# Performance work log

Measured on AMD Instinct MI355X. Metric: run time of the kernel, lower is better.

Reference implementation:

```python
import jax, jax.numpy as jnp
import numpy as np
from jax import lax

MID_NODES = 3
EMB = 128
NHID = 64
NHEADS = 8
ALPHA = 0.2
NEG_INF = -9e15


def build_adj(N, mid_nodes):
    # faithful numpy transcription of GATEmbedding.get_adj + row-normalize(adj + I)
    mid = (N - mid_nodes) // 2 + mid_nodes - 1
    width = (N - mid_nodes) // mid_nodes // 2
    A = np.zeros((N, N), dtype=np.float64)
    for i in range(mid_nodes):
        for j in range(N):
            if i == mid_nodes - 1:
                if j > mid_nodes - 1:
                    A[i, j] = 1
            elif j == i + 1 or (j > mid - (i + 1) * width and j < mid + (i + 1) * width):
                A[i, j] = 1
    for i in range(mid_nodes, N):
        for j in range(N):
            if i == mid_nodes:
                if j == mid_nodes + 1:
                    A[i, j] = 1
            elif i == N - 1:
                if j == N - 2:
                    A[i, j] = 1
            elif j == i - 1 or j == i + 1:
                A[i, j] = 1
    A = A + np.eye(N)
    rowsum = A.sum(1)
    r_inv = np.where(rowsum > 0, 1.0 / np.maximum(rowsum, 1e-30), 0.0)
    A = r_inv[:, None] * A
    return jnp.asarray(A, dtype=jnp.float32)


def conv2d(x, w, b):
    y = lax.conv_general_dilated(x, w, (1, 1), 'SAME',
                                 dimension_numbers=('NCHW', 'OIHW', 'NCHW'))
    return y + b[None, :, None, None]


def maxpool2(x):
    return lax.reduce_window(x, -jnp.inf, lax.max, (1, 1, 2, 2), (1, 1, 2, 2), 'VALID')


def slice_cnn(x, w1, b1, w2, b2, w3, b3, w4, b4, fc_w, fc_b):
    x = maxpool2(jax.nn.relu(conv2d(x, w1, b1)))
    x = maxpool2(jax.nn.relu(conv2d(x, w2, b2)))
    x = maxpool2(jax.nn.relu(conv2d(x, w3, b3)))
    x = maxpool2(jax.nn.relu(conv2d(x, w4, b4)))
    x = x.mean(axis=(2, 3))  # [BC,128]
    return x @ fc_w + fc_b


def setup_inputs():
    key = jax.random.key(0)
    ks = jax.random.split(key, 16)
    s = 0.05
    return {
        'input_img': jax.random.normal(ks[0], (8, 16, 128, 128), jnp.float32),
        'w1': jax.random.normal(ks[1], (32, 1, 3, 3), jnp.float32) * s,
        'b1': jnp.zeros((32,), jnp.float32),
        'w2': jax.random.normal(ks[2], (64, 32, 3, 3), jnp.float32) * s,
        'b2': jnp.zeros((64,), jnp.float32),
        'w3': jax.random.normal(ks[3], (128, 64, 3, 3), jnp.float32) * s,
        'b3': jnp.zeros((128,), jnp.float32),
        'w4': jax.random.normal(ks[4], (128, 128, 3, 3), jnp.float32) * s,
        'b4': jnp.zeros((128,), jnp.float32),
        'fc_cnn_w': jax.random.normal(ks[5], (128, EMB), jnp.float32) * s,
        'fc_cnn_b': jnp.zeros((EMB,), jnp.float32),
        'att_W': jax.random.normal(ks[6], (NHEADS, EMB, NHID), jnp.float32) * s,
        'att_a': jax.random.normal(ks[7], (NHEADS, 2 * NHID), jnp.float32) * s,
        'out_W': jax.random.normal(ks[8], (NHID * NHEADS, EMB), jnp.float32) * s,
        'out_a': jax.random.normal(ks[9], (2 * EMB,), jnp.float32) * s,
        'll_w': jax.random.normal(ks[10], (EMB, 2 * EMB), jnp.float32) * s,
        'll_b': jnp.zeros((2 * EMB,), jnp.float32),
        'fc_w': jax.random.normal(ks[11], (2 * EMB, 2), jnp.float32) * s,
        'fc_b': jnp.zeros((2,), jnp.float32),
        'sfc_w': jax.random.normal(ks[12], (EMB, 2), jnp.float32) * s,
        'sfc_b': jnp.zeros((2,), jnp.float32),
    }


def reference(input_img, w1, b1, w2, b2, w3, b3, w4, b4, fc_cnn_w, fc_cnn_b,
              att_W, att_a, out_W, out_a, ll_w, ll_b, fc_w, fc_b, sfc_w, sfc_b):
    B, C, H, W = input_img.shape
    N = C + MID_NODES

    # per-channel CNN embedding, batched over B*C instead of a Python loop
    feats = slice_cnn(input_img.reshape(B * C, 1, H, W),
                      w1, b1, w2, b2, w3, b3, w4, b4, fc_cnn_w, fc_cnn_b)
    feats = feats.reshape(B, C, EMB)                 # slices_features_stack
    slices_hidden = feats.mean(axis=1)               # [B,EMB]
    slices_out = slices_hidden @ sfc_w + sfc_b       # [B,2]

    slices = jnp.zeros((B, N, EMB), feats.dtype).at[:, MID_NODES:, :].set(feats)
    adj = build_adj(N, MID_NODES)                    # [N,N] constant
    mask = (adj > 0)[None, None]                     # [1,1,N,N]

    # multi-head GAT (eval mode: dropout = identity), all heads vectorized
    Wh = jnp.einsum('bnf,kfh->bknh', slices, att_W)  # [B,K,N,NHID]
    a1, a2 = att_a[:, :NHID], att_a[:, NHID:]
    e = jax.nn.leaky_relu(jnp.einsum('bknh,kh->bkn', Wh, a1)[:, :, :, None]
                          + jnp.einsum('bknh,kh->bkn', Wh, a2)[:, :, None, :], ALPHA)
    att = jax.nn.softmax(jnp.where(mask, e, NEG_INF), axis=-1)   # [B,K,N,N]
    batch_attention = att.mean(axis=1)               # [B,N,N]
    h = jnp.einsum('bkij,bkjh->bkih', att, Wh)
    x = jax.nn.elu(h).transpose(0, 2, 1, 3).reshape(B, N, NHEADS * NHID)

    # output GAT layer (concat=False), then external ELU
    Wh2 = x @ out_W                                   # [B,N,EMB]
    oa1, oa2 = out_a[:EMB], out_a[EMB:]
    e2 = jax.nn.leaky_relu((Wh2 @ oa1)[:, :, None] + (Wh2 @ oa2)[:, None, :], ALPHA)
    att2 = jax.nn.softmax(jnp.where(mask[:, 0], e2, NEG_INF), axis=-1)
    image_feature = jax.nn.elu(jnp.einsum('bij,bjh->bih', att2, Wh2))

    image_feature_second = image_feature[:, 0, :]
    image_feature_second = jax.nn.relu(image_feature_second @ ll_w + ll_b)
    prediction = image_feature_second @ fc_w + fc_b
    return (slices_hidden, image_feature_second, prediction, slices_out, batch_attention)
```

## Files before the change

kernel.cpp:

```cpp
#include <hip/hip_runtime.h>
#include <hip/hip_bf16.h>
#include <math.h>


#define NEG_INF_F (-9.0e15f)

typedef __attribute__((ext_vector_type(8))) short frag8;
typedef __attribute__((ext_vector_type(4))) float f32x4;
typedef const __attribute__((address_space(1))) void GasV;
typedef __attribute__((address_space(3))) void LasV;

__device__ __forceinline__ unsigned short f2bf(float f) {
  union { float f; unsigned u; } v; v.f = f;
  unsigned r = v.u + 0x7fffu + ((v.u >> 16) & 1u);
  return (unsigned short)(r >> 16);
}
__device__ __forceinline__ float bf2f(unsigned short u) {
  union { unsigned u; float f; } v; v.u = ((unsigned)u) << 16;
  return v.f;
}

template <int C>
__device__ __forceinline__ int swz(int slot, int px) {
  if constexpr (C == 32) return slot ^ ((px >> 1) & 3);
  else return slot ^ (px & 7);
}

template <int C, int OC>
__device__ __forceinline__ void bprep_dev(const float* __restrict__ w,
                                          unsigned short* __restrict__ bp, int idx) {
  constexpr int CS = C / 32, NSTEP = 9 * CS, NG = (OC / 64) * 2;
  if (idx >= NG * NSTEP * 64 * 2) return;
  int q = idx & 1;
  int lane = (idx >> 1) & 63;
  int gs = idx >> 7;
  int s = gs % NSTEP;
  int g = gs / NSTEP;
  int off = s / CS, c0 = (s % CS) * 32;
  int l15 = lane & 15, l4 = lane >> 4;
  int oc = (g >> 1) * 64 + (g & 1) * 32 + q * 16 + l15;
  int kc = c0 + l4 * 8;
  unsigned short o8[8];
#pragma unroll
  for (int j = 0; j < 8; ++j)
    o8[j] = f2bf(w[((size_t)oc * C + kc + j) * 9 + off]);
  *(uint4*)(bp + (size_t)idx * 8) = *(uint4*)o8;
}

__global__ __launch_bounds__(256) void prep_k(
    const float* __restrict__ w2, const float* __restrict__ w3,
    const float* __restrict__ w4, unsigned short* __restrict__ bp2,
    unsigned short* __restrict__ bp3, unsigned short* __restrict__ bp4,
    float* __restrict__ adj) {
  const int bx = blockIdx.x, t = threadIdx.x;
  if (bx == 0) {
    __shared__ float A[19][19];
    for (int e = t; e < 361; e += 256) {
      int i = e / 19, j = e % 19;
      float v = 0.f;
      const int MIDN = 3, N = 19, MID = 10, WIDTH = 2;
      if (i < MIDN) {
        if (i == MIDN - 1) { if (j > MIDN - 1) v = 1.f; }
        else if (j == i + 1 || (j > MID - (i + 1) * WIDTH && j < MID + (i + 1) * WIDTH)) v = 1.f;
      } else {
        if (i == MIDN) { if (j == MIDN + 1) v = 1.f; }
        else if (i == N - 1) { if (j == N - 2) v = 1.f; }
        else if (j == i - 1 || j == i + 1) v = 1.f;
      }
      if (i == j) v += 1.f;
      A[i][j] = v;
    }
    __syncthreads();
    for (int e = t; e < 361; e += 256) {
      int i = e / 19;
      float rs = 0.f;
      for (int j = 0; j < 19; ++j) rs += A[i][j];
      float rinv = rs > 0.f ? 1.f / rs : 0.f;
      adj[e] = A[i][e % 19] * rinv;
    }
  } else if (bx <= 9) {
    bprep_dev<32, 64>(w2, bp2, (bx - 1) * 256 + t);
  } else if (bx <= 45) {
    bprep_dev<64, 128>(w3, bp3, (bx - 10) * 256 + t);
  } else {
    bprep_dev<128, 128>(w4, bp4, (bx - 46) * 256 + t);
  }
}

__global__ __launch_bounds__(256) void conv12_k(
    const float* __restrict__ in, const float* __restrict__ w1,
    const float* __restrict__ b1, const unsigned short* __restrict__ bprep,
    const float* __restrict__ bias, unsigned short* __restrict__ outH) {
  constexpr int C = 32, OC = 64, W = 64;
  constexpr int PW = W + 2, OH = W / 2;
  constexpr int NSTEP = 9;
  __shared__ float sr[14][132];
  __shared__ __align__(16) unsigned short patchH[6 * PW * C];
  const int t = threadIdx.x;
  const int img = blockIdx.z;
  const int y0 = blockIdx.x * 4;
  const int pr0 = blockIdx.x * 2;
  const size_t out_img = (size_t)img * 34 * 34 * OC;

  const float* ip = in + (size_t)img * 16384;
  for (int e = t; e < 14 * 130; e += 256) {
    int s = e / 130, c = e - s * 130;
    int y = 2 * y0 - 3 + s, x = c - 1;
    sr[s][c] = (y >= 0 && y < 128 && x >= 0 && x < 128) ? ip[y * 128 + x] : 0.f;
  }
  __syncthreads();

  {
    const int px = t & 63, ocg = t >> 6;
    const int gx = px + 1;
    const int ssl = swz<C>(ocg, gx);
    const int ocg_s = __builtin_amdgcn_readfirstlane(ocg);
    const float* wg = w1 + ocg_s * 72;
    const float* bg = b1 + ocg_s * 8;
#pragma unroll
    for (int r = 0; r < 6; ++r) {
      int rp = y0 + r;
      unsigned short h8[8];
      if (rp == 0 || rp == 65) {
#pragma unroll
        for (int i = 0; i < 8; ++i) h8[i] = 0;
      } else {
        float v[4][4];
#pragma unroll
        for (int dy = 0; dy < 4; ++dy)
#pragma unroll
          for (int dx = 0; dx < 4; ++dx) v[dy][dx] = sr[2 * r + dy][2 * px + dx];
#pragma unroll
        for (int i = 0; i < 8; ++i) {
          float m = -1e30f;
#pragma unroll
          for (int dy = 0; dy < 2; ++dy)
#pragma unroll
            for (int dx = 0; dx < 2; ++dx) {
              float a = 0.f;
#pragma unroll
              for (int ky = 0; ky < 3; ++ky)
#pragma unroll
                for (int kx = 0; kx < 3; ++kx)
                  a = fmaf(v[dy + ky][dx + kx], wg[i * 9 + ky * 3 + kx], a);
              m = fmaxf(m, a);
            }
          h8[i] = f2bf(fmaxf(m + bg[i], 0.f));
        }
      }
      *(uint4*)(patchH + (r * PW + gx) * C + ssl * 8) = *(uint4*)h8;
    }
    if (t < 48) {
      int r = t >> 3, rem = t & 7;
      int side = rem >> 2, q = rem & 3;
      const uint4 z4 = {0u, 0u, 0u, 0u};
      *(uint4*)(patchH + (r * PW + side * (PW - 1)) * C + q * 8) = z4;
    }
  }
  __syncthreads();

  const int lane = t & 63, wid = t >> 6;
  const int wm = wid >> 1, wn = wid & 1;
  const int l15 = lane & 15, l4 = lane >> 4;
  const int nbase = wn * 32;
  const unsigned short* bpw = bprep + ((size_t)wn * NSTEP * 64 + lane) * 16;
  const float bb0 = bias[nbase + l15], bb1 = bias[nbase + 16 + l15];

#pragma unroll
  for (int tt = 0; tt < 2; ++tt) {
    f32x4 acc[4][2] = {};
    for (int s = 0; s < NSTEP; ++s) {
      const frag8* bp = (const frag8*)(bpw + (size_t)s * 1024);
      frag8 bh0 = bp[0], bh1 = bp[1];
      const int ky = s / 3, kx = s - ky * 3;
      frag8 ah[4];
#pragma unroll
      for (int f = 0; f < 4; ++f) {
        int m0 = wm * 32 + (f & 1) * 16 + (f >> 1) * 64;
        int ry = m0 / W + 2 * tt + ky;
        int px = (m0 % W) + l15 + kx;
        ah[f] = *(const frag8*)(patchH + ((size_t)ry * PW + px) * C + swz<C>(l4, px) * 8);
      }
#pragma unroll
      for (int f = 0; f < 4; ++f) {
        acc[f][0] = __builtin_amdgcn_mfma_f32_16x16x32_bf16(ah[f], bh0, acc[f][0], 0, 0, 0);
        acc[f][1] = __builtin_amdgcn_mfma_f32_16x16x32_bf16(ah[f], bh1, acc[f][1], 0, 0, 0);
      }
    }
#pragma unroll
    for (int pi = 0; pi < 2; ++pi) {
      const int fa = pi, fb = pi + 2;
      const int pxb = wm * 16 + pi * 8;
#pragma unroll
      for (int n = 0; n < 2; ++n) {
        const float bb = n ? bb1 : bb0;
#pragma unroll
        for (int xp = 0; xp < 2; ++xp) {
          float v = fmaxf(fmaxf(acc[fa][n][2 * xp], acc[fa][n][2 * xp + 1]),
                          fmaxf(acc[fb][n][2 * xp], acc[fb][n][2 * xp + 1]));
          outH[out_img + ((size_t)(pr0 + tt + 1) * 34 + pxb + 2 * l4 + xp + 1) * OC +
               nbase + n * 16 + l15] = f2bf(fmaxf(v + bb, 0.f));
        }
      }
    }
  }

  const uint4 z4 = {0u, 0u, 0u, 0u};
  if (t < 32) {
    int r = t >> 4, side = (t >> 3) & 1, q = t & 7;
    *(uint4*)(outH + out_img + ((size_t)(pr0 + r + 1) * 34 + side * 33) * OC + q * 8) = z4;
  }
  if (pr0 == 0)
    for (int e = t; e < 272; e += 256)
      *(uint4*)(outH + out_img + (size_t)e * 8) = z4;
  if (pr0 + 2 == OH)
    for (int e = t; e < 272; e += 256)
      *(uint4*)(outH + out_img + (size_t)33 * 34 * OC + (size_t)e * 8) = z4;
}

template <int C, int OC, int W, int R, bool PAD = true>
__global__ __launch_bounds__(256) void conv_mfma_k(
    const unsigned short* __restrict__ inH,
    const unsigned short* __restrict__ bprep, const float* __restrict__ bias,
    unsigned short* __restrict__ outH) {
  constexpr int SL = C / 8;
  constexpr int PW = W + 2;
  constexpr int OW = W / 2, OH = W / 2;
  constexpr int PR = R / 2;
  constexpr int CS = C / 32;
  constexpr int NSTEP = 9 * CS;
  constexpr int M = R * W;
  constexpr int MF = M / 32;
  constexpr int E = (R + 2) * PW * SL;
  constexpr int EP = (E + 63) & ~63;
  __shared__ __align__(16) unsigned short patchH[(R + 2) * PW * C + 256];
  const int t = threadIdx.x;
  const int img = blockIdx.z;
  const int y0 = blockIdx.x * R;
  const int pr0 = blockIdx.x * PR;
  const size_t in_img = (size_t)img * (W + 2) * (W + 2) * C;
  const size_t out_img = (size_t)img * (OW + 2) * (OW + 2) * OC;

  {
    const unsigned short* gH = inH + in_img + (size_t)y0 * PW * C;
    for (int e0 = t; e0 < EP; e0 += 256) {
      int e = e0 < E ? e0 : E - 1;
      int row = e / (PW * SL);
      int rem = e - row * (PW * SL);
      int px = rem / SL, sl = rem & (SL - 1);
      int goff = row * PW * C + px * C + swz<C>(sl, px) * 8;
      int lbase = __builtin_amdgcn_readfirstlane(e0 & ~63) * 8;
      __builtin_amdgcn_global_load_lds((GasV*)(gH + goff), (LasV*)(patchH + lbase), 16, 0, 0);
    }
  }
  __syncthreads();

  const int lane = t & 63, wid = t >> 6;
  const int wm = wid >> 1, wn = wid & 1;
  const int l15 = lane & 15, l4 = lane >> 4;
  const int nbase = wn * 64;

  f32x4 acc[MF][4] = {};
  const unsigned short* bpw0 =
      bprep + (((size_t)(wn * 2 + 0) * NSTEP) * 64 + lane) * 16;
  const unsigned short* bpw1 =
      bprep + (((size_t)(wn * 2 + 1) * NSTEP) * 64 + lane) * 16;

  for (int s = 0; s < NSTEP; ++s) {
    const frag8* bp0 = (const frag8*)(bpw0 + (size_t)s * 1024);
    const frag8* bp1 = (const frag8*)(bpw1 + (size_t)s * 1024);
    frag8 bh0 = bp0[0], bh1 = bp0[1], bh2 = bp1[0], bh3 = bp1[1];
    const int off = s / CS, c0 = (s % CS) * 32;
    const int ky = off / 3, kx = off - ky * 3;
    const int slin = (c0 >> 3) + l4;
    frag8 ah[MF];
#pragma unroll
    for (int f = 0; f < MF; ++f) {
      int m0 = wm * (M / 2) + f * 16;
      int ry = m0 / W + ky;
      int px = (m0 % W) + l15 + kx;
      ah[f] = *(const frag8*)(patchH + ((size_t)ry * PW + px) * C + swz<C>(slin, px) * 8);
    }
#pragma unroll
    for (int f = 0; f < MF; ++f) {
      acc[f][0] = __builtin_amdgcn_mfma_f32_16x16x32_bf16(ah[f], bh0, acc[f][0], 0, 0, 0);
      acc[f][1] = __builtin_amdgcn_mfma_f32_16x16x32_bf16(ah[f], bh1, acc[f][1], 0, 0, 0);
      acc[f][2] = __builtin_amdgcn_mfma_f32_16x16x32_bf16(ah[f], bh2, acc[f][2], 0, 0, 0);
      acc[f][3] = __builtin_amdgcn_mfma_f32_16x16x32_bf16(ah[f], bh3, acc[f][3], 0, 0, 0);
    }
  }

  float bb[4];
#pragma unroll
  for (int n = 0; n < 4; ++n) bb[n] = bias[nbase + n * 16 + l15];
#pragma unroll
  for (int pi = 0; pi < MF / 2; ++pi) {
    const int fa = (W == 16) ? (pi * 2) : pi;
    const int fb = (W == 16) ? (pi * 2 + 1) : (pi + 2);
    const int m0a = wm * (M / 2) + fa * 16;
    const int prow = (y0 + m0a / W) >> 1;
    const int pxb = (m0a % W) >> 1;
#pragma unroll
    for (int n = 0; n < 4; ++n) {
#pragma unroll
      for (int xp = 0; xp < 2; ++xp) {
        float v = fmaxf(fmaxf(acc[fa][n][2 * xp], acc[fa][n][2 * xp + 1]),
                        fmaxf(acc[fb][n][2 * xp], acc[fb][n][2 * xp + 1]));
        outH[out_img + ((size_t)(prow + 1) * (OW + 2) + pxb + 2 * l4 + xp + 1) * OC +
             nbase + n * 16 + l15] = f2bf(fmaxf(v + bb[n], 0.f));
      }
    }
  }

  if constexpr (PAD) {
    const uint4 z4 = {0u, 0u, 0u, 0u};
    if (t < PR * 32) {
      int r = t >> 5, rem = t & 31;
      int side = rem >> 4, q = rem & 15;
      *(uint4*)(outH + out_img + ((size_t)(pr0 + r + 1) * (OW + 2) + side * (OW + 1)) * OC +
                q * 8) = z4;
    }
    if (pr0 == 0)
      for (int e = t; e < (OW + 2) * 16; e += 256)
        *(uint4*)(outH + out_img + (size_t)(e >> 4) * OC + (e & 15) * 8) = z4;
    if (pr0 + PR == OH)
      for (int e = t; e < (OW + 2) * 16; e += 256)
        *(uint4*)(outH + out_img + ((size_t)(OH + 1) * (OW + 2) + (e >> 4)) * OC +
                  (e & 15) * 8) = z4;
  }
}

__global__ __launch_bounds__(128) void meanfc_k(
    const unsigned short* __restrict__ c4H, const float* __restrict__ fcw,
    const float* __restrict__ fcb, float* __restrict__ feats, int img0) {
  int img = blockIdx.x, t = threadIdx.x;
  __shared__ float sM[128];
  const unsigned short* pH = c4H + (size_t)img * 12800;
  float s0 = 0.f, s1 = 0.f;
  for (int pix = 0; pix < 64; pix += 2) {
    int py0 = pix >> 3, px0 = pix & 7;
    int py1 = (pix + 1) >> 3, px1 = (pix + 1) & 7;
    s0 += bf2f(pH[((size_t)(py0 + 1) * 10 + px0 + 1) * 128 + t]);
    s1 += bf2f(pH[((size_t)(py1 + 1) * 10 + px1 + 1) * 128 + t]);
  }
  sM[t] = (s0 + s1) * (1.f / 64.f);
  __syncthreads();
  float a0 = 0.f, a1 = 0.f, a2 = 0.f, a3 = 0.f;
  for (int c = 0; c < 128; c += 4) {
    a0 = fmaf(sM[c], fcw[c * 128 + t], a0);
    a1 = fmaf(sM[c + 1], fcw[(c + 1) * 128 + t], a1);
    a2 = fmaf(sM[c + 2], fcw[(c + 2) * 128 + t], a2);
    a3 = fmaf(sM[c + 3], fcw[(c + 3) * 128 + t], a3);
  }
  feats[(size_t)(img0 + img) * 128 + t] = fcb[t] + ((a0 + a1) + (a2 + a3));
}

__global__ __launch_bounds__(64) void wh_k(
    const float* __restrict__ feats, const float* __restrict__ attW,
    const float* __restrict__ atta, float* __restrict__ Wh,
    float* __restrict__ f1, float* __restrict__ f2) {
  int bid = blockIdx.x;
  int n = bid % 19;
  int k = (bid / 19) % 8;
  int b = bid / 152;
  int h = threadIdx.x;
  float acc = 0.f;
  if (n >= 3) {
    const float* s = feats + (size_t)(b * 16 + n - 3) * 128;
    const float* W = attW + (size_t)k * 8192 + h;
    float a0 = 0.f, a1 = 0.f, a2 = 0.f, a3 = 0.f;
    for (int f = 0; f < 128; f += 4) {
      a0 = fmaf(s[f], W[f * 64], a0);
      a1 = fmaf(s[f + 1], W[(f + 1) * 64], a1);
      a2 = fmaf(s[f + 2], W[(f + 2) * 64], a2);
      a3 = fmaf(s[f + 3], W[(f + 3) * 64], a3);
    }
    acc = (a0 + a1) + (a2 + a3);
  }
  Wh[(size_t)bid * 64 + h] = acc;
  float p1 = acc * atta[k * 128 + h];
  float p2 = acc * atta[k * 128 + 64 + h];
#pragma unroll
  for (int off = 32; off > 0; off >>= 1) {
    p1 += __shfl_down(p1, off);
    p2 += __shfl_down(p2, off);
  }
  if (h == 0) { f1[bid] = p1; f2[bid] = p2; }
}

__global__ __launch_bounds__(256) void gat1_k(
    const float* __restrict__ f1, const float* __restrict__ f2,
    const float* __restrict__ adj, const float* __restrict__ Wh,
    const float* __restrict__ feats, const float* __restrict__ sfcw,
    const float* __restrict__ sfcb, float* __restrict__ out,
    float* __restrict__ xb) {
  int b = blockIdx.x, t = threadIdx.x;
  __shared__ float satt[8][19][19];
  __shared__ float sadj[361], sf1[152], sf2[152];
  __shared__ float shh[128];
  for (int e = t; e < 361; e += 256) sadj[e] = adj[e];
  if (t < 152) { sf1[t] = f1[b * 152 + t]; sf2[t] = f2[b * 152 + t]; }
  __syncthreads();
  if (t < 152) {
    int k = t / 19, i = t % 19;
    float fi = sf1[t];
    float v[19];
    float mx = -1e30f;
#pragma unroll
    for (int j = 0; j < 19; ++j) {
      float e = fi + sf2[k * 19 + j];
      e = e >= 0.f ? e : 0.2f * e;
      e = sadj[i * 19 + j] > 0.f ? e : NEG_INF_F;
      v[j] = e;
      mx = fmaxf(mx, e);
    }
    float sum = 0.f;
#pragma unroll
    for (int j = 0; j < 19; ++j) { v[j] = expf(v[j] - mx); sum += v[j]; }
    float inv = 1.f / sum;
#pragma unroll
    for (int j = 0; j < 19; ++j) satt[k][i][j] = v[j] * inv;
  }
  __syncthreads();
  for (int e = t; e < 361; e += 256) {
    int i = e / 19, j = e - i * 19;
    float s = 0.f;
#pragma unroll
    for (int k = 0; k < 8; ++k) s += satt[k][i][j];
    out[3104 + b * 361 + e] = s * 0.125f;
  }
  int h = t & 63, g = t >> 6;
  for (int row = g; row < 152; row += 4) {
    int k = row / 19, i = row - k * 19;
    const float* whp = Wh + ((size_t)(b * 152 + k * 19)) * 64 + h;
    float s = 0.f;
#pragma unroll
    for (int j = 0; j < 19; ++j) s = fmaf(satt[k][i][j], whp[j * 64], s);
    xb[((size_t)b * 19 + i) * 512 + k * 64 + h] = s > 0.f ? s : expm1f(s);
  }
  if (t < 128) {
    float s = 0.f;
    for (int c = 0; c < 16; ++c) s += feats[(size_t)(b * 16 + c) * 128 + t];
    s *= (1.f / 16.f);
    out[b * 128 + t] = s;
    shh[t] = s;
  }
  __syncthreads();
  if (t < 2) {
    float a0 = 0.f, a1 = 0.f, a2 = 0.f, a3 = 0.f;
    for (int e = 0; e < 128; e += 4) {
      a0 = fmaf(shh[e], sfcw[e * 2 + t], a0);
      a1 = fmaf(shh[e + 1], sfcw[(e + 1) * 2 + t], a1);
      a2 = fmaf(shh[e + 2], sfcw[(e + 2) * 2 + t], a2);
      a3 = fmaf(shh[e + 3], sfcw[(e + 3) * 2 + t], a3);
    }
    out[3088 + b * 2 + t] = sfcb[t] + ((a0 + a1) + (a2 + a3));
  }
}

__global__ __launch_bounds__(128) void wh2_k(
    const float* __restrict__ xb, const float* __restrict__ outW,
    const float* __restrict__ oa, float* __restrict__ Wh2,
    float* __restrict__ o1, float* __restrict__ o2) {
  int bn = blockIdx.x, t = threadIdx.x;
  __shared__ float sx[512];
  __shared__ float r1[128], r2[128];
  for (int m = t; m < 512; m += 128) sx[m] = xb[(size_t)bn * 512 + m];
  __syncthreads();
  float a0 = 0.f, a1 = 0.f, a2 = 0.f, a3 = 0.f;
  for (int m = 0; m < 512; m += 4) {
    a0 = fmaf(sx[m], outW[m * 128 + t], a0);
    a1 = fmaf(sx[m + 1], outW[(m + 1) * 128 + t], a1);
    a2 = fmaf(sx[m + 2], outW[(m + 2) * 128 + t], a2);
    a3 = fmaf(sx[m + 3], outW[(m + 3) * 128 + t], a3);
  }
  float a = (a0 + a1) + (a2 + a3);
  Wh2[(size_t)bn * 128 + t] = a;
  r1[t] = a * oa[t];
  r2[t] = a * oa[128 + t];
  __syncthreads();
  for (int s = 64; s > 0; s >>= 1) {
    if (t < s) { r1[t] += r1[t + s]; r2[t] += r2[t + s]; }
    __syncthreads();
  }
  if (t == 0) { o1[bn] = r1[0]; o2[bn] = r2[0]; }
}

__global__ __launch_bounds__(256) void final_k(
    const float* __restrict__ adj, const float* __restrict__ o1,
    const float* __restrict__ o2, const float* __restrict__ Wh2,
    const float* __restrict__ llw, const float* __restrict__ llb,
    const float* __restrict__ fcw, const float* __restrict__ fcb,
    float* __restrict__ out) {
  int b = blockIdx.x, t = threadIdx.x;
  __shared__ float sA[19], sF[128], sG[256];
  if (t < 19) {
    float e = o1[b * 19] + o2[b * 19 + t];
    e = e >= 0.f ? e : 0.2f * e;
    sA[t] = adj[t] > 0.f ? e : NEG_INF_F;
  }
  __syncthreads();
  if (t == 0) {
    float mx = -1e30f;
    for (int j = 0; j < 19; ++j) mx = fmaxf(mx, sA[j]);
    float sum = 0.f;
    for (int j = 0; j < 19; ++j) { sA[j] = expf(sA[j] - mx); sum += sA[j]; }
    float inv = 1.f / sum;
    for (int j = 0; j < 19; ++j) sA[j] *= inv;
  }
  __syncthreads();
  if (t < 128) {
    float s = 0.f;
    for (int j = 0; j < 19; ++j) s = fmaf(sA[j], Wh2[(size_t)(b * 19 + j) * 128 + t], s);
    sF[t] = s > 0.f ? s : expm1f(s);
  }
  __syncthreads();
  {
    float a0 = 0.f, a1 = 0.f, a2 = 0.f, a3 = 0.f;
    for (int e = 0; e < 128; e += 4) {
      a0 = fmaf(sF[e], llw[e * 256 + t], a0);
      a1 = fmaf(sF[e + 1], llw[(e + 1) * 256 + t], a1);
      a2 = fmaf(sF[e + 2], llw[(e + 2) * 256 + t], a2);
      a3 = fmaf(sF[e + 3], llw[(e + 3) * 256 + t], a3);
    }
    float a = fmaxf(llb[t] + ((a0 + a1) + (a2 + a3)), 0.f);
    sG[t] = a;
    out[1024 + b * 256 + t] = a;
  }
  __syncthreads();
  if (t < 2) {
    float a0 = 0.f, a1 = 0.f, a2 = 0.f, a3 = 0.f;
    for (int o = 0; o < 256; o += 4) {
      a0 = fmaf(sG[o], fcw[o * 2 + t], a0);
      a1 = fmaf(sG[o + 1], fcw[(o + 1) * 2 + t], a1);
      a2 = fmaf(sG[o + 2], fcw[(o + 2) * 2 + t], a2);
      a3 = fmaf(sG[o + 3], fcw[(o + 3) * 2 + t], a3);
    }
    out[3072 + b * 2 + t] = fcb[t] + ((a0 + a1) + (a2 + a3));
  }
}

extern "C" void kernel_launch(void* const* d_in, const int* in_sizes, int n_in,
                              void* d_out, int out_size, void* d_ws, size_t ws_size,
                              hipStream_t stream) {
  const float* in_img   = (const float*)d_in[0];
  const float* w1       = (const float*)d_in[1];
  const float* b1       = (const float*)d_in[2];
  const float* w2       = (const float*)d_in[3];
  const float* b2       = (const float*)d_in[4];
  const float* w3       = (const float*)d_in[5];
  const float* b3       = (const float*)d_in[6];
  const float* w4       = (const float*)d_in[7];
  const float* b4       = (const float*)d_in[8];
  const float* fc_cnn_w = (const float*)d_in[9];
  const float* fc_cnn_b = (const float*)d_in[10];
  const float* att_W    = (const float*)d_in[11];
  const float* att_a    = (const float*)d_in[12];
  const float* out_W    = (const float*)d_in[13];
  const float* out_a    = (const float*)d_in[14];
  const float* ll_w     = (const float*)d_in[15];
  const float* ll_b     = (const float*)d_in[16];
  const float* fc_w     = (const float*)d_in[17];
  const float* fc_b     = (const float*)d_in[18];
  const float* sfc_w    = (const float*)d_in[19];
  const float* sfc_b    = (const float*)d_in[20];
  float* out = (float*)d_out;

  float* p = (float*)d_ws;
  float* adj   = p; p += 361;
  float* feats = p; p += 16384;
  float* Wh    = p; p += 77824;
  float* f1    = p; p += 1216;
  float* f2    = p; p += 1216;
  float* xb    = p; p += 77824;
  float* Wh2   = p; p += 19456;
  float* o1    = p; p += 152;
  float* o2    = p; p += 152;
  char* base = (char*)p;
  auto align16 = [&]() { base = (char*)(((uintptr_t)base + 15) & ~(uintptr_t)15); };
  align16();
  auto aus = [&](size_t n) { unsigned short* q = (unsigned short*)base; base += n * 2; return q; };
  unsigned short* bp2 = aus((size_t)2 * 9 * 64 * 2 * 8);
  unsigned short* bp3 = aus((size_t)4 * 18 * 64 * 2 * 8);
  unsigned short* bp4 = aus((size_t)4 * 36 * 64 * 2 * 8);
  align16();
  size_t fixed_bytes = (size_t)(base - (char*)d_ws);
  constexpr size_t PER_IMG_SH = 73984 + 41472 + 12800;
  int chunk = 128;
  while (chunk > 1 && fixed_bytes + (size_t)chunk * PER_IMG_SH * 2 > ws_size)
    chunk >>= 1;
  unsigned short* buf2H = (unsigned short*)base;
  unsigned short* buf3H = buf2H + (size_t)chunk * 73984;
  unsigned short* buf4H = buf3H + (size_t)chunk * 41472;

  prep_k<<<118, 256, 0, stream>>>(w2, w3, w4, bp2, bp3, bp4, adj);

  for (int c0 = 0; c0 < 128; c0 += chunk) {
    conv12_k<<<dim3(16, 1, chunk), 256, 0, stream>>>(
        in_img + (size_t)c0 * 16384, w1, b1, bp2, b2, buf2H);
    conv_mfma_k<64, 128, 32, 4><<<dim3(8, 1, chunk), 256, 0, stream>>>(
        buf2H, bp3, b3, buf3H);
    conv_mfma_k<128, 128, 16, 4, false><<<dim3(4, 1, chunk), 256, 0, stream>>>(
        buf3H, bp4, b4, buf4H);
    meanfc_k<<<chunk, 128, 0, stream>>>(buf4H, fc_cnn_w, fc_cnn_b, feats, c0);
  }

  wh_k<<<1216, 64, 0, stream>>>(feats, att_W, att_a, Wh, f1, f2);
  gat1_k<<<8, 256, 0, stream>>>(f1, f2, adj, Wh, feats, sfc_w, sfc_b, out, xb);
  wh2_k<<<152, 128, 0, stream>>>(xb, out_W, out_a, Wh2, o1, o2);
  final_k<<<8, 256, 0, stream>>>(adj, o1, o2, Wh2, ll_w, ll_b, fc_w, fc_b, out);
}
```

Before: 141.4 us.

## Fuse conv4 pooling into per-row partial sums and merge meanfc with Wh projection

The last conv stage now reduces its pooled ReLU outputs directly into per-row channel partial sums instead of writing a padded bf16 feature map. A new kernel combines the mean, the CNN fc and the per-head GAT Wh/f1/f2 projection for each image, which removes the separate wh_k launch. The rows of Wh, f1 and f2 for the mid nodes are zeroed in prep_k. This cuts global traffic and one kernel launch, at the cost of a heavier per-image tail kernel with fewer blocks.

```diff
diff --git a/kernel.cpp b/kernel.cpp
--- a/kernel.cpp
+++ b/kernel.cpp
@@ -51,7 +51,8 @@
     const float* __restrict__ w2, const float* __restrict__ w3,
     const float* __restrict__ w4, unsigned short* __restrict__ bp2,
     unsigned short* __restrict__ bp3, unsigned short* __restrict__ bp4,
-    float* __restrict__ adj) {
+    float* __restrict__ adj, float* __restrict__ Wh,
+    float* __restrict__ f1, float* __restrict__ f2) {
   const int bx = blockIdx.x, t = threadIdx.x;
   if (bx == 0) {
     __shared__ float A[19][19];
@@ -78,12 +79,23 @@
       float rinv = rs > 0.f ? 1.f / rs : 0.f;
       adj[e] = A[i][e % 19] * rinv;
     }
-  } else if (bx <= 9) {
-    bprep_dev<32, 64>(w2, bp2, (bx - 1) * 256 + t);
-  } else if (bx <= 45) {
-    bprep_dev<64, 128>(w3, bp3, (bx - 10) * 256 + t);
+  } else if (bx == 1) {
+    for (int e = t; e < 12288; e += 256) {
+      int row = e >> 6;
+      int b = row / 24, rem = row - b * 24, k = rem / 3, n = rem - k * 3;
+      Wh[((size_t)(b * 152 + k * 19 + n)) * 64 + (e & 63)] = 0.f;
+    }
+    if (t < 192) {
+      int b = t / 24, rem = t - b * 24, k = rem / 3, n = rem - k * 3;
+      f1[b * 152 + k * 19 + n] = 0.f;
+      f2[b * 152 + k * 19 + n] = 0.f;
+    }
+  } else if (bx <= 10) {
+    bprep_dev<32, 64>(w2, bp2, (bx - 2) * 256 + t);
+  } else if (bx <= 46) {
+    bprep_dev<64, 128>(w3, bp3, (bx - 11) * 256 + t);
   } else {
-    bprep_dev<128, 128>(w4, bp4, (bx - 46) * 256 + t);
+    bprep_dev<128, 128>(w4, bp4, (bx - 47) * 256 + t);
   }
 }
 
@@ -218,7 +230,7 @@
       *(uint4*)(outH + out_img + (size_t)33 * 34 * OC + (size_t)e * 8) = z4;
 }
 
-template <int C, int OC, int W, int R, bool PAD = true>
+template <int C, int OC, int W, int R>
 __global__ __launch_bounds__(256) void conv_mfma_k(
     const unsigned short* __restrict__ inH,
     const unsigned short* __restrict__ bprep, const float* __restrict__ bias,
@@ -312,80 +324,191 @@
     }
   }
 
-  if constexpr (PAD) {
-    const uint4 z4 = {0u, 0u, 0u, 0u};
-    if (t < PR * 32) {
-      int r = t >> 5, rem = t & 31;
-      int side = rem >> 4, q = rem & 15;
-      *(uint4*)(outH + out_img + ((size_t)(pr0 + r + 1) * (OW + 2) + side * (OW + 1)) * OC +
-                q * 8) = z4;
-    }
-    if (pr0 == 0)
-      for (int e = t; e < (OW + 2) * 16; e += 256)
-        *(uint4*)(outH + out_img + (size_t)(e >> 4) * OC + (e & 15) * 8) = z4;
-    if (pr0 + PR == OH)
-      for (int e = t; e < (OW + 2) * 16; e += 256)
-        *(uint4*)(outH + out_img + ((size_t)(OH + 1) * (OW + 2) + (e >> 4)) * OC +
-                  (e & 15) * 8) = z4;
-  }
-}
-
-__global__ __launch_bounds__(128) void meanfc_k(
-    const unsigned short* __restrict__ c4H, const float* __restrict__ fcw,
-    const float* __restrict__ fcb, float* __restrict__ feats, int img0) {
-  int img = blockIdx.x, t = threadIdx.x;
-  __shared__ float sM[128];
-  const unsigned short* pH = c4H + (size_t)img * 12800;
-  float s0 = 0.f, s1 = 0.f;
-  for (int pix = 0; pix < 64; pix += 2) {
-    int py0 = pix >> 3, px0 = pix & 7;
-    int py1 = (pix + 1) >> 3, px1 = (pix + 1) & 7;
-    s0 += bf2f(pH[((size_t)(py0 + 1) * 10 + px0 + 1) * 128 + t]);
-    s1 += bf2f(pH[((size_t)(py1 + 1) * 10 + px1 + 1) * 128 + t]);
-  }
-  sM[t] = (s0 + s1) * (1.f / 64.f);
-  __syncthreads();
-  float a0 = 0.f, a1 = 0.f, a2 = 0.f, a3 = 0.f;
-  for (int c = 0; c < 128; c += 4) {
-    a0 = fmaf(sM[c], fcw[c * 128 + t], a0);
-    a1 = fmaf(sM[c + 1], fcw[(c + 1) * 128 + t], a1);
-    a2 = fmaf(sM[c + 2], fcw[(c + 2) * 128 + t], a2);
-    a3 = fmaf(sM[c + 3], fcw[(c + 3) * 128 + t], a3);
-  }
-  feats[(size_t)(img0 + img) * 128 + t] = fcb[t] + ((a0 + a1) + (a2 + a3));
-}
-
-__global__ __launch_bounds__(64) void wh_k(
-    const float* __restrict__ feats, const float* __restrict__ attW,
-    const float* __restrict__ atta, float* __restrict__ Wh,
-    float* __restrict__ f1, float* __restrict__ f2) {
-  int bid = blockIdx.x;
-  int n = bid % 19;
-  int k = (bid / 19) % 8;
-  int b = bid / 152;
-  int h = threadIdx.x;
-  float acc = 0.f;
-  if (n >= 3) {
-    const float* s = feats + (size_t)(b * 16 + n - 3) * 128;
-    const float* W = attW + (size_t)k * 8192 + h;
+  const uint4 z4 = {0u, 0u, 0u, 0u};
+  if (t < PR * 32) {
+    int r = t >> 5, rem = t & 31;
+    int side = rem >> 4, q = rem & 15;
+    *(uint4*)(outH + out_img + ((size_t)(pr0 + r + 1) * (OW + 2) + side * (OW + 1)) * OC +
+              q * 8) = z4;
+  }
+  if (pr0 == 0)
+    for (int e = t; e < (OW + 2) * 16; e += 256)
+      *(uint4*)(outH + out_img + (size_t)(e >> 4) * OC + (e & 15) * 8) = z4;
+  if (pr0 + PR == OH)
+    for (int e = t; e < (OW + 2) * 16; e += 256)
+      *(uint4*)(outH + out_img + ((size_t)(OH + 1) * (OW + 2) + (e >> 4)) * OC +
+                (e & 15) * 8) = z4;
+}
+
+__global__ __launch_bounds__(256) void conv4_psum_k(
+    const unsigned short* __restrict__ inH,
+    const unsigned short* __restrict__ bprep, const float* __restrict__ bias,
+    float* __restrict__ psum) {
+  constexpr int C = 128, OC = 128, W = 16, R = 4;
+  constexpr int SL = C / 8;
+  constexpr int PW = W + 2;
+  constexpr int CS = C / 32;
+  constexpr int NSTEP = 9 * CS;
+  constexpr int M = R * W;
+  constexpr int MF = M / 32;
+  constexpr int E = (R + 2) * PW * SL;
+  constexpr int EP = (E + 63) & ~63;
+  __shared__ __align__(16) unsigned short patchH[(R + 2) * PW * C + 256];
+  const int t = threadIdx.x;
+  const int img = blockIdx.z;
+  const int y0 = blockIdx.x * R;
+  const size_t in_img = (size_t)img * (W + 2) * (W + 2) * C;
+
+  {
+    const unsigned short* gH = inH + in_img + (size_t)y0 * PW * C;
+    for (int e0 = t; e0 < EP; e0 += 256) {
+      int e = e0 < E ? e0 : E - 1;
+      int row = e / (PW * SL);
+      int rem = e - row * (PW * SL);
+      int px = rem / SL, sl = rem & (SL - 1);
+      int goff = row * PW * C + px * C + swz<C>(sl, px) * 8;
+      int lbase = __builtin_amdgcn_readfirstlane(e0 & ~63) * 8;
+      __builtin_amdgcn_global_load_lds((GasV*)(gH + goff), (LasV*)(patchH + lbase), 16, 0, 0);
+    }
+  }
+  __syncthreads();
+
+  const int lane = t & 63, wid = t >> 6;
+  const int wm = wid >> 1, wn = wid & 1;
+  const int l15 = lane & 15, l4 = lane >> 4;
+  const int nbase = wn * 64;
+
+  f32x4 acc[MF][4] = {};
+  const unsigned short* bpw0 =
+      bprep + (((size_t)(wn * 2 + 0) * NSTEP) * 64 + lane) * 16;
+  const unsigned short* bpw1 =
+      bprep + (((size_t)(wn * 2 + 1) * NSTEP) * 64 + lane) * 16;
+
+  for (int s = 0; s < NSTEP; ++s) {
+    const frag8* bp0 = (const frag8*)(bpw0 + (size_t)s * 1024);
+    const frag8* bp1 = (const frag8*)(bpw1 + (size_t)s * 1024);
+    frag8 bh0 = bp0[0], bh1 = bp0[1], bh2 = bp1[0], bh3 = bp1[1];
+    const int off = s / CS, c0 = (s % CS) * 32;
+    const int ky = off / 3, kx = off - ky * 3;
+    const int slin = (c0 >> 3) + l4;
+    frag8 ah[MF];
+#pragma unroll
+    for (int f = 0; f < MF; ++f) {
+      int m0 = wm * (M / 2) + f * 16;
+      int ry = m0 / W + ky;
+      int px = (m0 % W) + l15 + kx;
+      ah[f] = *(const frag8*)(patchH + ((size_t)ry * PW + px) * C + swz<C>(slin, px) * 8);
+    }
+#pragma unroll
+    for (int f = 0; f < MF; ++f) {
+      acc[f][0] = __builtin_amdgcn_mfma_f32_16x16x32_bf16(ah[f], bh0, acc[f][0], 0, 0, 0);
+      acc[f][1] = __builtin_amdgcn_mfma_f32_16x16x32_bf16(ah[f], bh1, acc[f][1], 0, 0, 0);
+      acc[f][2] = __builtin_amdgcn_mfma_f32_16x16x32_bf16(ah[f], bh2, acc[f][2], 0, 0, 0);
+      acc[f][3] = __builtin_amdgcn_mfma_f32_16x16x32_bf16(ah[f], bh3, acc[f][3], 0, 0, 0);
+    }
+  }
+
+  const int prow = blockIdx.x * 2 + wm;
+  float sums[4];
+#pragma unroll
+  for (int n = 0; n < 4; ++n) {
+    const float bb = bias[nbase + n * 16 + l15];
+    float s = 0.f;
+#pragma unroll
+    for (int xp = 0; xp < 2; ++xp) {
+      float v = fmaxf(fmaxf(acc[0][n][2 * xp], acc[0][n][2 * xp + 1]),
+                      fmaxf(acc[1][n][2 * xp], acc[1][n][2 * xp + 1]));
+      s += fmaxf(v + bb, 0.f);
+    }
+    s += __shfl_xor(s, 16);
+    s += __shfl_xor(s, 32);
+    sums[n] = s;
+  }
+  if (l4 == 0) {
+#pragma unroll
+    for (int n = 0; n < 4; ++n)
+      psum[(size_t)img * 1024 + prow * 128 + nbase + n * 16 + l15] = sums[n];
+  }
+}
+
+__global__ __launch_bounds__(128) void meanwh_k(
+    const float* __restrict__ psum, const float* __restrict__ fcw,
+    const float* __restrict__ fcb, const float* __restrict__ attW,
+    const float* __restrict__ atta, float* __restrict__ feats,
+    float* __restrict__ Wh, float* __restrict__ f1, float* __restrict__ f2,
+    int img0) {
+  const int img = blockIdx.x, t = threadIdx.x;
+  const int gimg = img0 + img;
+  __shared__ float sM[128], sF[128], sW[512], r1[128], r2[128];
+  {
+    const float* ps = psum + (size_t)img * 1024;
+    float s = 0.f;
+#pragma unroll
+    for (int r = 0; r < 8; ++r) s += ps[r * 128 + t];
+    sM[t] = s * (1.f / 64.f);
+  }
+  __syncthreads();
+  {
     float a0 = 0.f, a1 = 0.f, a2 = 0.f, a3 = 0.f;
-    for (int f = 0; f < 128; f += 4) {
-      a0 = fmaf(s[f], W[f * 64], a0);
-      a1 = fmaf(s[f + 1], W[(f + 1) * 64], a1);
-      a2 = fmaf(s[f + 2], W[(f + 2) * 64], a2);
-      a3 = fmaf(s[f + 3], W[(f + 3) * 64], a3);
-    }
-    acc = (a0 + a1) + (a2 + a3);
-  }
-  Wh[(size_t)bid * 64 + h] = acc;
-  float p1 = acc * atta[k * 128 + h];
-  float p2 = acc * atta[k * 128 + 64 + h];
-#pragma unroll
-  for (int off = 32; off > 0; off >>= 1) {
-    p1 += __shfl_down(p1, off);
-    p2 += __shfl_down(p2, off);
-  }
-  if (h == 0) { f1[bid] = p1; f2[bid] = p2; }
+    for (int c = 0; c < 128; c += 4) {
+      a0 = fmaf(sM[c], fcw[c * 128 + t], a0);
+      a1 = fmaf(sM[c + 1], fcw[(c + 1) * 128 + t], a1);
+      a2 = fmaf(sM[c + 2], fcw[(c + 2) * 128 + t], a2);
+      a3 = fmaf(sM[c + 3], fcw[(c + 3) * 128 + t], a3);
+    }
+    float v = fcb[t] + ((a0 + a1) + (a2 + a3));
+    feats[(size_t)gimg * 128 + t] = v;
+    sF[t] = v;
+  }
+  __syncthreads();
+  const int b = gimg >> 4;
+  const int n = (gimg & 15) + 3;
+  {
+    const int h = t & 63;
+    const int kb = t >> 6;
+    float c0 = 0.f, c1 = 0.f, c2 = 0.f, c3 = 0.f;
+    const float* W0 = attW + (size_t)(kb + 0) * 8192 + h;
+    const float* W1 = attW + (size_t)(kb + 2) * 8192 + h;
+    const float* W2 = attW + (size_t)(kb + 4) * 8192 + h;
+    const float* W3 = attW + (size_t)(kb + 6) * 8192 + h;
+    for (int f = 0; f < 128; ++f) {
+      float sf = sF[f];
+      c0 = fmaf(sf, W0[f * 64], c0);
+      c1 = fmaf(sf, W1[f * 64], c1);
+      c2 = fmaf(sf, W2[f * 64], c2);
+      c3 = fmaf(sf, W3[f * 64], c3);
+    }
+    sW[(kb + 0) * 64 + h] = c0;
+    sW[(kb + 2) * 64 + h] = c1;
+    sW[(kb + 4) * 64 + h] = c2;
+    sW[(kb + 6) * 64 + h] = c3;
+    Wh[((size_t)(b * 152 + (kb + 0) * 19 + n)) * 64 + h] = c0;
+    Wh[((size_t)(b * 152 + (kb + 2) * 19 + n)) * 64 + h] = c1;
+    Wh[((size_t)(b * 152 + (kb + 4) * 19 + n)) * 64 + h] = c2;
+    Wh[((size_t)(b * 152 + (kb + 6) * 19 + n)) * 64 + h] = c3;
+  }
+  __syncthreads();
+  {
+    const int k = t >> 4, part = t & 15;
+    float p1 = 0.f, p2 = 0.f;
+#pragma unroll
+    for (int i = 0; i < 4; ++i) {
+      int h = part * 4 + i;
+      float w = sW[k * 64 + h];
+      p1 = fmaf(w, atta[k * 128 + h], p1);
+      p2 = fmaf(w, atta[k * 128 + 64 + h], p2);
+    }
+    r1[t] = p1;
+    r2[t] = p2;
+  }
+  __syncthreads();
+  if (t < 8) {
+    float s1 = 0.f, s2 = 0.f;
+#pragma unroll
+    for (int i = 0; i < 16; ++i) { s1 += r1[t * 16 + i]; s2 += r2[t * 16 + i]; }
+    f1[b * 152 + t * 19 + n] = s1;
+    f2[b * 152 + t * 19 + n] = s2;
+  }
 }
 
 __global__ __launch_bounds__(256) void gat1_k(
@@ -576,6 +699,7 @@
   float* Wh2   = p; p += 19456;
   float* o1    = p; p += 152;
   float* o2    = p; p += 152;
+  float* psum  = p; p += 131072;
   char* base = (char*)p;
   auto align16 = [&]() { base = (char*)(((uintptr_t)base + 15) & ~(uintptr_t)15); };
   align16();
@@ -585,27 +709,25 @@
   unsigned short* bp4 = aus((size_t)4 * 36 * 64 * 2 * 8);
   align16();
   size_t fixed_bytes = (size_t)(base - (char*)d_ws);
-  constexpr size_t PER_IMG_SH = 73984 + 41472 + 12800;
+  constexpr size_t PER_IMG_SH = 73984 + 41472;
   int chunk = 128;
   while (chunk > 1 && fixed_bytes + (size_t)chunk * PER_IMG_SH * 2 > ws_size)
     chunk >>= 1;
   unsigned short* buf2H = (unsigned short*)base;
   unsigned short* buf3H = buf2H + (size_t)chunk * 73984;
-  unsigned short* buf4H = buf3H + (size_t)chunk * 41472;
-
-  prep_k<<<118, 256, 0, stream>>>(w2, w3, w4, bp2, bp3, bp4, adj);
+
+  prep_k<<<119, 256, 0, stream>>>(w2, w3, w4, bp2, bp3, bp4, adj, Wh, f1, f2);
 
   for (int c0 = 0; c0 < 128; c0 += chunk) {
     conv12_k<<<dim3(16, 1, chunk), 256, 0, stream>>>(
         in_img + (size_t)c0 * 16384, w1, b1, bp2, b2, buf2H);
     conv_mfma_k<64, 128, 32, 4><<<dim3(8, 1, chunk), 256, 0, stream>>>(
         buf2H, bp3, b3, buf3H);
-    conv_mfma_k<128, 128, 16, 4, false><<<dim3(4, 1, chunk), 256, 0, stream>>>(
-        buf3H, bp4, b4, buf4H);
-    meanfc_k<<<chunk, 128, 0, stream>>>(buf4H, fc_cnn_w, fc_cnn_b, feats, c0);
-  }
-
-  wh_k<<<1216, 64, 0, stream>>>(feats, att_W, att_a, Wh, f1, f2);
+    conv4_psum_k<<<dim3(4, 1, chunk), 256, 0, stream>>>(buf3H, bp4, b4, psum);
+    meanwh_k<<<chunk, 128, 0, stream>>>(psum, fc_cnn_w, fc_cnn_b, att_W, att_a,
+                                        feats, Wh, f1, f2, c0);
+  }
+
   gat1_k<<<8, 256, 0, stream>>>(f1, f2, adj, Wh, feats, sfc_w, sfc_b, out, xb);
   wh2_k<<<152, 128, 0, stream>>>(xb, out_W, out_a, Wh2, o1, o2);
   final_k<<<8, 256, 0, stream>>>(adj, o1, o2, Wh2, ll_w, ll_b, fc_w, fc_b, out);
```

After: 143.2 us. Within noise of the previous version (+1.3%).
